# Optimization experiments

Hardware: AMD Instinct MI355X
Metric: run time of the kernel (lower is better)

## Reference

```python
import jax, jax.numpy as jnp
import numpy as np

N_NODES = 100000
N_EDGES = 3200000
B = 64            # number of graphs / RNA batch
DIM = 16          # GINE hidden dim
NFP = 33          # protein node feature dim
EMB = 128         # embedding dim
MAXLEN = 3000     # rna_global length (conv1d in_channels)
LOCLEN = 2998     # rna_local length = 3000 - log4(64) + 1
NF = 32           # n_filters
KS = 8            # conv kernel size -> 128-8+1 = 121
FC_IN = NF * 121  # 3872
BN_EPS = 1e-5


def setup_inputs() -> dict:
    key = jax.random.key(0)
    ks = jax.random.split(key, 32)
    s = 0.1
    p = {}
    # forward data args
    p['pro_x'] = jax.random.normal(ks[0], (N_NODES, NFP), jnp.float32)
    p['pro_edge_index'] = jax.random.randint(ks[1], (2, N_EDGES), 0, N_NODES, jnp.int32)
    p['pro_weight'] = jax.random.uniform(ks[2], (N_EDGES, 1), jnp.float32)
    p['pro_batch'] = jnp.sort(jax.random.randint(ks[3], (N_NODES,), 0, B, jnp.int32))
    p['rna_global'] = jax.random.randint(ks[4], (B, MAXLEN), 0, 5, jnp.int32)
    p['rna_local'] = jax.random.randint(ks[5], (B, LOCLEN), 0, 65, jnp.int32)
    # GINE layer 1 (33 -> 16)
    p['g1_w1'] = jax.random.normal(ks[6], (NFP, DIM), jnp.float32) * s
    p['g1_b1'] = jnp.zeros((DIM,), jnp.float32)
    p['g1_w2'] = jax.random.normal(ks[7], (DIM, DIM), jnp.float32) * s
    p['g1_b2'] = jnp.zeros((DIM,), jnp.float32)
    p['g1_ew'] = jax.random.normal(ks[8], (1, NFP), jnp.float32) * s  # edge Linear(1, 33)
    p['g1_eb'] = jnp.zeros((NFP,), jnp.float32)
    p['g1_eps'] = jnp.zeros((), jnp.float32)
    # GINE layers 2-5 (16 -> 16), stacked on leading axis
    p['g_w1'] = jax.random.normal(ks[9], (4, DIM, DIM), jnp.float32) * s
    p['g_b1'] = jnp.zeros((4, DIM), jnp.float32)
    p['g_w2'] = jax.random.normal(ks[10], (4, DIM, DIM), jnp.float32) * s
    p['g_b2'] = jnp.zeros((4, DIM), jnp.float32)
    p['g_ew'] = jax.random.normal(ks[11], (4, 1, DIM), jnp.float32) * s  # edge Linear(1, 16)
    p['g_eb'] = jnp.zeros((4, DIM), jnp.float32)
    p['g_eps'] = jnp.zeros((4,), jnp.float32)
    # BatchNorm1d x5
    p['bn_gamma'] = jnp.ones((5, DIM), jnp.float32)
    p['bn_beta'] = jnp.zeros((5, DIM), jnp.float32)
    # fc1_xp (16 -> 128)
    p['fc1_xp_w'] = jax.random.normal(ks[12], (DIM, EMB), jnp.float32) * s
    p['fc1_xp_b'] = jnp.zeros((EMB,), jnp.float32)
    # RNA branch
    p['emb1'] = jax.random.normal(ks[13], (5, EMB), jnp.float32)
    p['emb2'] = jax.random.normal(ks[14], (65, EMB), jnp.float32)
    p['convr1_w'] = jax.random.normal(ks[15], (NF, MAXLEN, KS), jnp.float32) * 0.01
    p['convr1_b'] = jnp.zeros((NF,), jnp.float32)
    p['convr2_w'] = jax.random.normal(ks[16], (NF, LOCLEN, KS), jnp.float32) * 0.01
    p['convr2_b'] = jnp.zeros((NF,), jnp.float32)
    p['fcxr_w'] = jax.random.normal(ks[17], (FC_IN, EMB), jnp.float32) * 0.01
    p['fcxr_b'] = jnp.zeros((EMB,), jnp.float32)
    return p


def _gine(x, src, dst, ew, w1, b1, w2, b2, ew_w, ew_b, eps):
    # GINEConv: out = MLP((1+eps)*x + sum_j relu(x_j + edge_lin(e_ij)))
    e = ew @ ew_w + ew_b                       # [E, d]
    m = jax.nn.relu(x[src] + e)                # [E, d] gather + fuse
    agg = jax.ops.segment_sum(m, dst, num_segments=N_NODES)
    h = (1.0 + eps) * x + agg
    return jax.nn.relu(h @ w1 + b1) @ w2 + b2


def _bn(x, gamma, beta):
    mu = jnp.mean(x, axis=0)
    var = jnp.var(x, axis=0)
    return (x - mu) * jax.lax.rsqrt(var + BN_EPS) * gamma + beta


def _rna_branch(tokens, emb, cw, cb, fcw, fcb):
    x = emb[tokens]                            # [B, L, 128]
    y = jax.lax.conv_general_dilated(x, cw, (1,), 'VALID',
                                     dimension_numbers=('NCH', 'OIH', 'NCH'))
    y = y + cb[None, :, None]                  # [B, 32, 121]
    return y.reshape(y.shape[0], -1) @ fcw + fcb


def reference(pro_x, pro_edge_index, pro_weight, pro_batch, rna_global, rna_local,
              g1_w1, g1_b1, g1_w2, g1_b2, g1_ew, g1_eb, g1_eps,
              g_w1, g_b1, g_w2, g_b2, g_ew, g_eb, g_eps,
              bn_gamma, bn_beta, fc1_xp_w, fc1_xp_b,
              emb1, emb2, convr1_w, convr1_b, convr2_w, convr2_b, fcxr_w, fcxr_b):
    src, dst = pro_edge_index[0], pro_edge_index[1]
    # RNA global / local branches (shared fc_xr)
    xrg = _rna_branch(rna_global, emb1, convr1_w, convr1_b, fcxr_w, fcxr_b)
    xrl = _rna_branch(rna_local, emb2, convr2_w, convr2_b, fcxr_w, fcxr_b)
    # protein GINE stack
    xp = jax.nn.relu(_gine(pro_x, src, dst, pro_weight,
                           g1_w1, g1_b1, g1_w2, g1_b2, g1_ew, g1_eb, g1_eps))
    xp = _bn(xp, bn_gamma[0], bn_beta[0])
    for i in range(4):
        xp = jax.nn.relu(_gine(xp, src, dst, pro_weight,
                               g_w1[i], g_b1[i], g_w2[i], g_b2[i],
                               g_ew[i], g_eb[i], g_eps[i]))
        xp = _bn(xp, bn_gamma[i + 1], bn_beta[i + 1])
    # global mean pool over graphs
    sums = jax.ops.segment_sum(xp, pro_batch, num_segments=B)
    cnt = jax.ops.segment_sum(jnp.ones((N_NODES, 1), xp.dtype), pro_batch, num_segments=B)
    xp = jax.nn.relu((sums / jnp.maximum(cnt, 1.0)) @ fc1_xp_w + fc1_xp_b)
    # dropout in eval mode -> identity
    xc_rna = 0.5 * (xrg + xrl)
    return (xc_rna, xp)
```

## Files before the change

kernel.cpp:

```cpp
#include <hip/hip_runtime.h>
#include <hip/hip_fp16.h>

#define N_NODES 100000
#define N_EDGES 3200000
#define BGR 64
#define DIM 16
#define NFP 33
#define ROW1 32
#define H1STR 36
#define EMB 128
#define MAXLEN 3000
#define LOCLEN 2998
#define NF 32
#define KS 8
#define OUTT 121
#define FC_IN 3872
#define BN_EPSV 1e-5f
#define POOL_CHUNK 256
#define POOL_BLKS 391
#define MLPB 391
#define AGGB1 6250
#define AGGB16 3125
#define NBIN 391
#define BCNT_BLK 512
#define P1_CHUNK 4096
#define P1_BLOCKS 782
#define MAXBIN 9088
#define NKC 32
#define KCH 121
#define WDEC (1.f / 32767.f)

__global__ void __launch_bounds__(256) k_bincnt(const int* __restrict__ dst,
                                                int* __restrict__ bh) {
    __shared__ int hist[NBIN];
    int t = threadIdx.x, bid = blockIdx.x;
    for (int b = t; b < NBIN; b += 256) hist[b] = 0;
    __syncthreads();
    int e0 = bid * (N_EDGES / BCNT_BLK);
    int e1 = e0 + (N_EDGES / BCNT_BLK);
    for (int e = e0 + t; e < e1; e += 256) atomicAdd(&hist[dst[e] >> 8], 1);
    __syncthreads();
    for (int b = t; b < NBIN; b += 256) bh[b * BCNT_BLK + bid] = hist[b];
}

__global__ void __launch_bounds__(512) k_binscan(const int* __restrict__ bh,
                                                 int* __restrict__ binoff,
                                                 int* __restrict__ bincur) {
    __shared__ int sc[512];
    int t = threadIdx.x;
    int s = 0;
    if (t < NBIN) {
        const int* row = bh + t * BCNT_BLK;
        for (int k = 0; k < BCNT_BLK; k++) s += row[k];
    }
    sc[t] = s;
    __syncthreads();
    for (int off = 1; off < 512; off <<= 1) {
        int v = (t >= off) ? sc[t - off] : 0;
        __syncthreads();
        sc[t] += v;
        __syncthreads();
    }
    int excl = sc[t] - s;
    if (t <= NBIN) binoff[t] = excl;
    if (t < NBIN) bincur[t] = excl;
}

__global__ void __launch_bounds__(256) k_part1(const int* __restrict__ src,
                                               const int* __restrict__ dst,
                                               const float* __restrict__ w,
                                               int* __restrict__ bincur,
                                               int2* __restrict__ tmp_sw) {
    __shared__ int2 srec[P1_CHUNK];
    __shared__ unsigned short sbin[P1_CHUNK];
    __shared__ unsigned short sperm[P1_CHUNK];
    __shared__ int hist[NBIN];
    __shared__ int off[NBIN];
    __shared__ int cur[NBIN];
    __shared__ int base[NBIN];
    __shared__ int sc[512];
    int t = threadIdx.x;
    int g0 = blockIdx.x * P1_CHUNK;
    int cn = N_EDGES - g0; if (cn > P1_CHUNK) cn = P1_CHUNK;
    for (int b = t; b < NBIN; b += 256) hist[b] = 0;
    __syncthreads();
    for (int j = t; j < cn; j += 256) {
        int d = dst[g0 + j];
        int b = d >> 8;
        sbin[j] = (unsigned short)b;
        srec[j] = make_int2(src[g0 + j] | ((d & 255) << 20), __float_as_int(w[g0 + j]));
        atomicAdd(&hist[b], 1);
    }
    __syncthreads();
    sc[t] = (t < NBIN) ? hist[t] : 0;
    sc[256 + t] = (256 + t < NBIN) ? hist[256 + t] : 0;
    __syncthreads();
    for (int o = 1; o <= 256; o <<= 1) {
        int v0 = (t >= o) ? sc[t - o] : 0;
        int v1 = sc[256 + t - o];
        __syncthreads();
        sc[t] += v0;
        sc[256 + t] += v1;
        __syncthreads();
    }
    for (int b = t; b < NBIN; b += 256) {
        int e = sc[b] - hist[b];
        off[b] = e;
        cur[b] = e;
        int c = hist[b];
        base[b] = c ? atomicAdd(&bincur[b], c) : 0;
    }
    __syncthreads();
    for (int j = t; j < cn; j += 256) {
        int p = atomicAdd(&cur[sbin[j]], 1);
        sperm[p] = (unsigned short)j;
    }
    __syncthreads();
    for (int p = t; p < cn; p += 256) {
        int j = sperm[p];
        int b = sbin[j];
        tmp_sw[base[b] + (p - off[b])] = srec[j];
    }
}

__global__ void __launch_bounds__(256) k_part2(const int2* __restrict__ tmp_sw,
                                               const int* __restrict__ binoff,
                                               unsigned* __restrict__ er,
                                               int* __restrict__ ptr) {
    __shared__ unsigned char sdl[MAXBIN];
    __shared__ unsigned short perm[MAXBIN];
    __shared__ int hist[256];
    __shared__ int cur[256];
    __shared__ int sc[256];
    int t = threadIdx.x, b = blockIdx.x;
    int nlo = b << 8;
    int e0 = binoff[b], e1 = binoff[b + 1];
    int cnt = e1 - e0;
    int stage = cnt < MAXBIN ? cnt : MAXBIN;
    hist[t] = 0;
    __syncthreads();
    for (int j = t; j < stage; j += 256) {
        unsigned char dl = (unsigned char)((tmp_sw[e0 + j].x >> 20) & 255);
        sdl[j] = dl;
        atomicAdd(&hist[dl], 1);
    }
    for (int j = stage + t; j < cnt; j += 256)
        atomicAdd(&hist[(tmp_sw[e0 + j].x >> 20) & 255], 1);
    __syncthreads();
    int v = hist[t];
    sc[t] = v;
    __syncthreads();
    for (int off = 1; off < 256; off <<= 1) {
        int u = (t >= off) ? sc[t - off] : 0;
        __syncthreads();
        sc[t] += u;
        __syncthreads();
    }
    int excl = sc[t] - v;
    cur[t] = excl;
    if (nlo + t < N_NODES) ptr[nlo + t] = e0 + excl;
    if (b == NBIN - 1 && t == 0) ptr[N_NODES] = N_EDGES;
    __syncthreads();
    for (int j = t; j < stage; j += 256) {
        int p = atomicAdd(&cur[sdl[j]], 1);
        perm[p] = (unsigned short)j;
    }
    __syncthreads();
    for (int j = stage + t; j < cnt; j += 256) {
        int2 sw = tmp_sw[e0 + j];
        int p = atomicAdd(&cur[(sw.x >> 20) & 255], 1);
        unsigned wq = (unsigned)(__int_as_float(sw.y) * 32767.f + 0.5f);
        er[e0 + p] = ((unsigned)sw.x & 0x1FFFFu) | (wq << 17);
    }
    for (int p = t; p < stage; p += 256) {
        int2 sw = tmp_sw[e0 + perm[p]];
        unsigned wq = (unsigned)(__int_as_float(sw.y) * 32767.f + 0.5f);
        er[e0 + p] = ((unsigned)sw.x & 0x1FFFFu) | (wq << 17);
    }
}

__global__ void k_half1(const float* __restrict__ x, __half* __restrict__ xh,
                        __half* __restrict__ xh32) {
    int i = blockIdx.x * blockDim.x + threadIdx.x;
    if (i < N_NODES * NFP) {
        int n = i / NFP, f = i - n * NFP;
        __half v = __float2half(x[i]);
        if (f < 32) xh[n * ROW1 + f] = v;
        else xh32[n] = v;
    }
}

__device__ __forceinline__ void acc8p(float a[8], uint4 r, float wv,
                                      const float* __restrict__ ewf,
                                      const float* __restrict__ ebf) {
    float2 f01 = __half22float2(*(__half2*)&r.x);
    float2 f23 = __half22float2(*(__half2*)&r.y);
    float2 f45 = __half22float2(*(__half2*)&r.z);
    float2 f67 = __half22float2(*(__half2*)&r.w);
    float x[8] = {f01.x, f01.y, f23.x, f23.y, f45.x, f45.y, f67.x, f67.y};
    #pragma unroll
    for (int j = 0; j < 8; j++)
        a[j] += fmaxf(x[j] + fmaf(wv, ewf[j], ebf[j]), 0.f);
}

__device__ __forceinline__ void acc8s(float a[8], uint4 r, float wv,
                                      const float* __restrict__ scf,
                                      const float* __restrict__ cbf,
                                      const float* __restrict__ ewf) {
    float2 f01 = __half22float2(*(__half2*)&r.x);
    float2 f23 = __half22float2(*(__half2*)&r.y);
    float2 f45 = __half22float2(*(__half2*)&r.z);
    float2 f67 = __half22float2(*(__half2*)&r.w);
    float x[8] = {f01.x, f01.y, f23.x, f23.y, f45.x, f45.y, f67.x, f67.y};
    #pragma unroll
    for (int j = 0; j < 8; j++)
        a[j] += fmaxf(fmaf(x[j], scf[j], fmaf(wv, ewf[j], cbf[j])), 0.f);
}

__global__ void __launch_bounds__(256) k_agg1(
    const __half* __restrict__ xh, const __half* __restrict__ xh32,
    const int* __restrict__ ptr, const unsigned* __restrict__ er,
    const float* __restrict__ ew, const float* __restrict__ ebv,
    const float* __restrict__ epsp, float* __restrict__ h) {
    int t = threadIdx.x;
    int wave = t >> 6, lane = t & 63;
    int nl = lane >> 4;
    int slot = (lane >> 2) & 3;
    int q = lane & 3;
    float ewf[8], ebf[8];
    #pragma unroll
    for (int j = 0; j < 8; j++) { ewf[j] = ew[q * 8 + j]; ebf[j] = ebv[q * 8 + j]; }
    float ew32 = ew[32], eb32 = ebv[32];
    float ep = 1.f + epsp[0];
    int node = blockIdx.x * 16 + wave * 4 + nl;
    int e0 = ptr[node], e1 = ptr[node + 1];
    float a[8] = {0, 0, 0, 0, 0, 0, 0, 0};
    float a32 = 0.f;
    int i = e0 + slot;
    while (i + 4 < e1) {
        unsigned ev0 = er[i];
        unsigned ev1 = er[i + 4];
        int s0 = ev0 & 0x1FFFF, s1 = ev1 & 0x1FFFF;
        float wv0 = (float)(ev0 >> 17) * WDEC;
        float wv1 = (float)(ev1 >> 17) * WDEC;
        uint4 r0 = *(const uint4*)(xh + s0 * ROW1 + q * 8);
        uint4 r1 = *(const uint4*)(xh + s1 * ROW1 + q * 8);
        acc8p(a, r0, wv0, ewf, ebf);
        acc8p(a, r1, wv1, ewf, ebf);
        if (q == 0) {
            a32 += fmaxf(__half2float(xh32[s0]) + fmaf(wv0, ew32, eb32), 0.f);
            a32 += fmaxf(__half2float(xh32[s1]) + fmaf(wv1, ew32, eb32), 0.f);
        }
        i += 8;
    }
    if (i < e1) {
        unsigned ev = er[i];
        int s = ev & 0x1FFFF;
        float wv = (float)(ev >> 17) * WDEC;
        uint4 r = *(const uint4*)(xh + s * ROW1 + q * 8);
        acc8p(a, r, wv, ewf, ebf);
        if (q == 0)
            a32 += fmaxf(__half2float(xh32[s]) + fmaf(wv, ew32, eb32), 0.f);
    }
    #pragma unroll
    for (int j = 0; j < 8; j++) {
        a[j] += __shfl_xor(a[j], 4);
        a[j] += __shfl_xor(a[j], 8);
    }
    a32 += __shfl_xor(a32, 4);
    a32 += __shfl_xor(a32, 8);
    if (slot == 0) {
        uint4 sraw = *(const uint4*)(xh + node * ROW1 + q * 8);
        float2 s01 = __half22float2(*(__half2*)&sraw.x);
        float2 s23 = __half22float2(*(__half2*)&sraw.y);
        float2 s45 = __half22float2(*(__half2*)&sraw.z);
        float2 s67 = __half22float2(*(__half2*)&sraw.w);
        float* hp = h + node * H1STR + q * 8;
        *(float4*)hp = make_float4(ep * s01.x + a[0], ep * s01.y + a[1],
                                   ep * s23.x + a[2], ep * s23.y + a[3]);
        *(float4*)(hp + 4) = make_float4(ep * s45.x + a[4], ep * s45.y + a[5],
                                         ep * s67.x + a[6], ep * s67.y + a[7]);
        if (q == 0)
            h[node * H1STR + 32] = ep * __half2float(xh32[node]) + a32;
    }
}

__global__ void __launch_bounds__(256) k_agg16(
    const __half* __restrict__ zh, const int* __restrict__ ptr,
    const unsigned* __restrict__ er,
    const float* __restrict__ ew, const float* __restrict__ ebv,
    const float* __restrict__ epsp,
    const float* __restrict__ bnstat, const float* __restrict__ gamma,
    const float* __restrict__ beta, float* __restrict__ h) {
    int t = threadIdx.x;
    int wave = t >> 6, lane = t & 63;
    int nl = lane >> 3;
    int slot = (lane >> 1) & 3;
    int hh = lane & 1;
    float ep = 1.f + epsp[0];
    const float invn = 1.f / (float)N_NODES;
    float scf[8], shf[8], cbf[8], ewf[8];
    #pragma unroll
    for (int j = 0; j < 8; j++) {
        int f = hh * 8 + j;
        float mu = bnstat[f] * invn;
        float var = bnstat[DIM + f] * invn - mu * mu;
        float sc = gamma[f] * rsqrtf(var + BN_EPSV);
        scf[j] = sc;
        shf[j] = beta[f] - mu * sc;
        cbf[j] = shf[j] + ebv[f];
        ewf[j] = ew[f];
    }
    int node = blockIdx.x * 32 + wave * 8 + nl;
    int e0 = ptr[node], e1 = ptr[node + 1];
    float a[8] = {0, 0, 0, 0, 0, 0, 0, 0};
    int i = e0 + slot;
    while (i + 4 < e1) {
        unsigned ev0 = er[i];
        unsigned ev1 = er[i + 4];
        float wv0 = (float)(ev0 >> 17) * WDEC;
        float wv1 = (float)(ev1 >> 17) * WDEC;
        uint4 r0 = *(const uint4*)(zh + (ev0 & 0x1FFFFu) * DIM + hh * 8);
        uint4 r1 = *(const uint4*)(zh + (ev1 & 0x1FFFFu) * DIM + hh * 8);
        acc8s(a, r0, wv0, scf, cbf, ewf);
        acc8s(a, r1, wv1, scf, cbf, ewf);
        i += 8;
    }
    if (i < e1) {
        unsigned ev = er[i];
        float wv = (float)(ev >> 17) * WDEC;
        uint4 r = *(const uint4*)(zh + (ev & 0x1FFFFu) * DIM + hh * 8);
        acc8s(a, r, wv, scf, cbf, ewf);
    }
    #pragma unroll
    for (int j = 0; j < 8; j++) a[j] += __shfl_xor(a[j], 2);
    #pragma unroll
    for (int j = 0; j < 8; j++) a[j] += __shfl_xor(a[j], 4);
    if (slot == 0) {
        uint4 sraw = *(const uint4*)(zh + node * DIM + hh * 8);
        float2 s01 = __half22float2(*(__half2*)&sraw.x);
        float2 s23 = __half22float2(*(__half2*)&sraw.y);
        float2 s45 = __half22float2(*(__half2*)&sraw.z);
        float2 s67 = __half22float2(*(__half2*)&sraw.w);
        float xs[8] = {s01.x, s01.y, s23.x, s23.y, s45.x, s45.y, s67.x, s67.y};
        float o8[8];
        #pragma unroll
        for (int j = 0; j < 8; j++)
            o8[j] = ep * fmaf(xs[j], scf[j], shf[j]) + a[j];
        float* hp = h + node * DIM + hh * 8;
        *(float4*)hp = make_float4(o8[0], o8[1], o8[2], o8[3]);
        *(float4*)(hp + 4) = make_float4(o8[4], o8[5], o8[6], o8[7]);
    }
}

__device__ __forceinline__ void mlp_bn_tail(float zv[16], bool active, int t,
                                            float* __restrict__ part) {
    __shared__ float red[4][32];
    float zs[16], zq[16];
    #pragma unroll
    for (int o = 0; o < 16; o++) {
        zs[o] = active ? zv[o] : 0.f;
        zq[o] = active ? zv[o] * zv[o] : 0.f;
    }
    #pragma unroll
    for (int m = 1; m <= 32; m <<= 1) {
        #pragma unroll
        for (int o = 0; o < 16; o++) {
            zs[o] += __shfl_xor(zs[o], m);
            zq[o] += __shfl_xor(zq[o], m);
        }
    }
    int wave = t >> 6, lane = t & 63;
    if (lane == 0) {
        #pragma unroll
        for (int o = 0; o < 16; o++) {
            red[wave][o] = zs[o];
            red[wave][16 + o] = zq[o];
        }
    }
    __syncthreads();
    if (t < 32)
        part[blockIdx.x * 32 + t] = red[0][t] + red[1][t] + red[2][t] + red[3][t];
}

__device__ __forceinline__ void store_zh(__half* __restrict__ zh, int n, float zv[16]) {
    __half2 p[8];
    #pragma unroll
    for (int j = 0; j < 8; j++) p[j] = __floats2half2_rn(zv[2 * j], zv[2 * j + 1]);
    *(uint4*)(zh + n * DIM) = *(uint4*)&p[0];
    *(uint4*)(zh + n * DIM + 8) = *(uint4*)&p[4];
}

__global__ void __launch_bounds__(256) k_mlp16(
    const float* __restrict__ h,
    const float* __restrict__ W1, const float* __restrict__ b1,
    const float* __restrict__ W2, const float* __restrict__ b2,
    __half* __restrict__ zh, float* __restrict__ part) {
    __shared__ float W1s[256], W2s[256], b1s[16], b2s[16];
    int t = threadIdx.x;
    W1s[t] = W1[t];
    W2s[t] = W2[t];
    if (t < 16) { b1s[t] = b1[t]; b2s[t] = b2[t]; }
    __syncthreads();
    int n = blockIdx.x * 256 + t;
    bool active = n < N_NODES;
    float zv[16];
    if (active) {
        float hv[16];
        #pragma unroll
        for (int j = 0; j < 4; j++) {
            float4 v = *(const float4*)(h + n * DIM + j * 4);
            hv[j * 4] = v.x; hv[j * 4 + 1] = v.y; hv[j * 4 + 2] = v.z; hv[j * 4 + 3] = v.w;
        }
        float tv[16];
        #pragma unroll
        for (int o = 0; o < 16; o++) {
            float s = b1s[o];
            #pragma unroll
            for (int f = 0; f < 16; f++) s += hv[f] * W1s[f * 16 + o];
            tv[o] = fmaxf(s, 0.f);
        }
        #pragma unroll
        for (int o = 0; o < 16; o++) {
            float s = b2s[o];
            #pragma unroll
            for (int f = 0; f < 16; f++) s += tv[f] * W2s[f * 16 + o];
            zv[o] = fmaxf(s, 0.f);
        }
        store_zh(zh, n, zv);
    }
    mlp_bn_tail(zv, active, t, part);
}

__global__ void __launch_bounds__(256) k_mlp1(
    const float* __restrict__ h,
    const float* __restrict__ W1, const float* __restrict__ b1,
    const float* __restrict__ W2, const float* __restrict__ b2,
    __half* __restrict__ zh, float* __restrict__ part) {
    __shared__ float W1s[NFP * 16], W2s[256], b1s[16], b2s[16];
    int t = threadIdx.x;
    for (int j = t; j < NFP * 16; j += 256) W1s[j] = W1[j];
    W2s[t] = W2[t];
    if (t < 16) { b1s[t] = b1[t]; b2s[t] = b2[t]; }
    __syncthreads();
    int n = blockIdx.x * 256 + t;
    bool active = n < N_NODES;
    float zv[16];
    if (active) {
        float hv[NFP];
        #pragma unroll
        for (int j = 0; j < 8; j++) {
            float4 v = *(const float4*)(h + n * H1STR + j * 4);
            hv[j * 4] = v.x; hv[j * 4 + 1] = v.y; hv[j * 4 + 2] = v.z; hv[j * 4 + 3] = v.w;
        }
        hv[32] = h[n * H1STR + 32];
        float tv[16];
        #pragma unroll
        for (int o = 0; o < 16; o++) {
            float s = b1s[o];
            #pragma unroll
            for (int f = 0; f < NFP; f++) s += hv[f] * W1s[f * 16 + o];
            tv[o] = fmaxf(s, 0.f);
        }
        #pragma unroll
        for (int o = 0; o < 16; o++) {
            float s = b2s[o];
            #pragma unroll
            for (int f = 0; f < 16; f++) s += tv[f] * W2s[f * 16 + o];
            zv[o] = fmaxf(s, 0.f);
        }
        store_zh(zh, n, zv);
    }
    mlp_bn_tail(zv, active, t, part);
}

__global__ void __launch_bounds__(1024) k_bnred(const float* __restrict__ part,
                                                float* __restrict__ bnstat) {
    __shared__ float red[1024];
    int t = threadIdx.x;
    int f = t & 31, g = t >> 5;
    float s = 0.f;
    for (int i = g; i < MLPB; i += 32) s += part[i * 32 + f];
    red[t] = s;
    __syncthreads();
    for (int off = 512; off >= 32; off >>= 1) {
        if (t < off) red[t] += red[t + off];
        __syncthreads();
    }
    if (t < 32) bnstat[t] = red[t];
}

__global__ void __launch_bounds__(256) k_pool(const __half* __restrict__ zh,
                                              const int* __restrict__ batch,
                                              const float* __restrict__ bnstat,
                                              const float* __restrict__ gamma,
                                              const float* __restrict__ beta,
                                              float* __restrict__ gsum,
                                              float* __restrict__ gcnt) {
    __shared__ float lsum[BGR * DIM];
    __shared__ float lcnt[BGR];
    int t = threadIdx.x;
    for (int j = t; j < BGR * DIM; j += 256) lsum[j] = 0.f;
    if (t < BGR) lcnt[t] = 0.f;
    __syncthreads();
    int f = t & 15, r = t >> 4;
    const float invn = 1.f / (float)N_NODES;
    float mu = bnstat[f] * invn;
    float var = bnstat[DIM + f] * invn - mu * mu;
    float sc = gamma[f] * rsqrtf(var + BN_EPSV);
    float sh = beta[f] - mu * sc;
    int start = blockIdx.x * POOL_CHUNK;
    float acc = 0.f, cacc = 0.f;
    int cur = -1;
    for (int i = 0; i < POOL_CHUNK / 16; i++) {
        int n = start + r + i * 16;
        if (n >= N_NODES) break;
        int b = batch[n];
        if (b != cur) {
            if (cur >= 0) {
                atomicAdd(&lsum[cur * DIM + f], acc);
                if (f == 0) atomicAdd(&lcnt[cur], cacc);
            }
            cur = b; acc = 0.f; cacc = 0.f;
        }
        acc += fmaf(__half2float(zh[n * DIM + f]), sc, sh);
        cacc += 1.f;
    }
    if (cur >= 0) {
        atomicAdd(&lsum[cur * DIM + f], acc);
        if (f == 0) atomicAdd(&lcnt[cur], cacc);
    }
    __syncthreads();
    for (int j = t; j < BGR * DIM; j += 256) {
        float v = lsum[j];
        if (v != 0.f) atomicAdd(&gsum[j], v);
    }
    if (t < BGR) {
        float v = lcnt[t];
        if (v != 0.f) atomicAdd(&gcnt[t], v);
    }
}

__global__ void k_xp(const float* __restrict__ gsum, const float* __restrict__ gcnt,
                     const float* __restrict__ w, const float* __restrict__ bias,
                     float* __restrict__ out) {
    int b = blockIdx.x;
    int e = threadIdx.x;
    float inv = 1.f / fmaxf(gcnt[b], 1.f);
    float acc = bias[e];
    #pragma unroll
    for (int f = 0; f < DIM; f++) acc += gsum[b * DIM + f] * inv * w[f * EMB + e];
    out[b * EMB + e] = fmaxf(acc, 0.f);
}

__global__ void __launch_bounds__(256) k_bucket(const int* __restrict__ tok, int L, int V,
                                                int* __restrict__ blist,
                                                int* __restrict__ bptr) {
    __shared__ int hist[65];
    __shared__ int cursor[65];
    int b = blockIdx.x, t = threadIdx.x;
    if (t < V) hist[t] = 0;
    __syncthreads();
    for (int l = t; l < L; l += 256) atomicAdd(&hist[tok[b * L + l]], 1);
    __syncthreads();
    if (t == 0) {
        int run = 0;
        for (int v = 0; v < V; v++) {
            cursor[v] = run;
            bptr[b * (V + 1) + v] = run;
            run += hist[v];
        }
        bptr[b * (V + 1) + V] = run;
    }
    __syncthreads();
    for (int l = t; l < L; l += 256) {
        int v = tok[b * L + l];
        int p = atomicAdd(&cursor[v], 1);
        blist[b * L + p] = l;
    }
}

__global__ void __launch_bounds__(256) k_wsum(const int* __restrict__ blist,
                                              const int* __restrict__ bptr,
                                              const float* __restrict__ cw,
                                              float* __restrict__ W, int L, int V) {
    int b = blockIdx.x, v = blockIdx.y;
    int t = threadIdx.x, o = t >> 3, k = t & 7;
    int s = bptr[b * (V + 1) + v], e = bptr[b * (V + 1) + v + 1];
    __shared__ int tk[256];
    const float* cwp = cw + o * (L * KS) + k;
    float acc = 0.f;
    for (int j0 = s; j0 < e; j0 += 256) {
        int lim = e - j0; if (lim > 256) lim = 256;
        __syncthreads();
        if (t < lim) tk[t] = blist[b * L + j0 + t];
        __syncthreads();
        for (int j = 0; j < lim; j++) acc += cwp[tk[j] * KS];
    }
    W[((b * NF + o) * V + v) * KS + k] = acc;
}

__global__ void k_y(const float* __restrict__ Wg, const float* __restrict__ Wl,
                    const float* __restrict__ emb1, const float* __restrict__ emb2,
                    const float* __restrict__ cb1, const float* __restrict__ cb2,
                    float* __restrict__ yg, float* __restrict__ yl) {
    int which = blockIdx.y;
    int bo = blockIdx.x;
    int b = bo >> 5, o = bo & 31;
    int t = threadIdx.x;
    const float* W = which ? Wl : Wg;
    const float* emb = which ? emb2 : emb1;
    const float* cb = which ? cb2 : cb1;
    float* y = which ? yl : yg;
    int V = which ? 65 : 5;
    __shared__ float Wsh[65 * KS];
    const float* Wrow = W + (b * NF + o) * V * KS;
    for (int j = t; j < V * KS; j += 128) Wsh[j] = Wrow[j];
    __syncthreads();
    if (t < OUTT) {
        float acc = cb[o];
        for (int v = 0; v < V; v++) {
            const float* ep = emb + v * EMB + t;
            #pragma unroll
            for (int k = 0; k < KS; k++) acc += Wsh[v * KS + k] * ep[k];
        }
        y[(b * NF + o) * OUTT + t] = acc;
    }
}

__global__ void __launch_bounds__(128) k_fcpart(const float* __restrict__ yg,
                                                const float* __restrict__ yl,
                                                const float* __restrict__ w,
                                                float* __restrict__ partial) {
    int b = blockIdx.x, which = blockIdx.y, kc = blockIdx.z;
    const float* y = which ? yl : yg;
    int e = threadIdx.x;
    __shared__ float ych[KCH];
    int j0 = kc * KCH;
    if (e < KCH) ych[e] = y[b * FC_IN + j0 + e];
    __syncthreads();
    float acc = 0.f;
    #pragma unroll 4
    for (int jj = 0; jj < KCH; jj++) acc += ych[jj] * w[(j0 + jj) * EMB + e];
    partial[((which * BGR + b) * NKC + kc) * EMB + e] = acc;
}

__global__ void k_fcred(const float* __restrict__ partial, const float* __restrict__ bias,
                        float* __restrict__ out) {
    int b = blockIdx.x;
    int e = threadIdx.x;
    const float* pg = partial + b * NKC * EMB + e;
    const float* pl = partial + (BGR + b) * NKC * EMB + e;
    float ag = bias[e], al = bias[e];
    #pragma unroll
    for (int k = 0; k < NKC; k++) { ag += pg[k * EMB]; al += pl[k * EMB]; }
    out[b * EMB + e] = 0.5f * (ag + al);
}

extern "C" void kernel_launch(void* const* d_in, const int* in_sizes, int n_in,
                              void* d_out, int out_size, void* d_ws, size_t ws_size,
                              hipStream_t stream) {
    const float* pro_x = (const float*)d_in[0];
    const int* eidx = (const int*)d_in[1];
    const int* esrc = eidx;
    const int* edst = eidx + N_EDGES;
    const float* pw = (const float*)d_in[2];
    const int* batch = (const int*)d_in[3];
    const int* rg = (const int*)d_in[4];
    const int* rl = (const int*)d_in[5];
    const float* g1_w1 = (const float*)d_in[6];
    const float* g1_b1 = (const float*)d_in[7];
    const float* g1_w2 = (const float*)d_in[8];
    const float* g1_b2 = (const float*)d_in[9];
    const float* g1_ew = (const float*)d_in[10];
    const float* g1_eb = (const float*)d_in[11];
    const float* g1_eps = (const float*)d_in[12];
    const float* g_w1 = (const float*)d_in[13];
    const float* g_b1 = (const float*)d_in[14];
    const float* g_w2 = (const float*)d_in[15];
    const float* g_b2 = (const float*)d_in[16];
    const float* g_ew = (const float*)d_in[17];
    const float* g_eb = (const float*)d_in[18];
    const float* g_eps = (const float*)d_in[19];
    const float* bn_gamma = (const float*)d_in[20];
    const float* bn_beta = (const float*)d_in[21];
    const float* fc1_xp_w = (const float*)d_in[22];
    const float* fc1_xp_b = (const float*)d_in[23];
    const float* emb1 = (const float*)d_in[24];
    const float* emb2 = (const float*)d_in[25];
    const float* convr1_w = (const float*)d_in[26];
    const float* convr1_b = (const float*)d_in[27];
    const float* convr2_w = (const float*)d_in[28];
    const float* convr2_b = (const float*)d_in[29];
    const float* fcxr_w = (const float*)d_in[30];
    const float* fcxr_b = (const float*)d_in[31];
    float* out = (float*)d_out;

    float* wsf = (float*)d_ws;
    int* ptr       = (int*)wsf;        wsf += 100128;
    int* binoff    = (int*)wsf;        wsf += 512;
    int* bincur    = (int*)wsf;        wsf += 512;
    unsigned* er   = (unsigned*)wsf;   wsf += 2 * N_EDGES;
    float* stats   = wsf;              wsf += 1280;
    float* un = wsf;
    int2* tmp_sw          = (int2*)un;
    int* bh               = (int*)(un + 7200000);
    __half* zh   = (__half*)(un + 1600000);
    __half* xh1  = (__half*)(un + 2400000);
    __half* xh32 = (__half*)(un + 4000000);
    float* bpart = un + 4100000;
    float* Wg    = un + 4300000;
    float* Wl    = un + 4382000;
    float* yg    = un + 5447000;
    float* yl    = un + 5695000;
    int* blg     = (int*)(un + 5961000);
    int* bll     = (int*)(un + 6153000);
    int* bpg     = (int*)(un + 6345000);
    int* bpl     = (int*)(un + 6346000);
    float* fcpart = un + 6360000;
    float* h      = un + 7400000;
    float* gsum   = stats;
    float* gcnt   = stats + 1024;
    float* bnstat = stats + 1088;

    hipMemsetAsync(stats, 0, 1280 * sizeof(float), stream);

    k_bincnt<<<BCNT_BLK, 256, 0, stream>>>(edst, bh);
    k_binscan<<<1, 512, 0, stream>>>(bh, binoff, bincur);
    k_part1<<<P1_BLOCKS, 256, 0, stream>>>(esrc, edst, pw, bincur, tmp_sw);
    k_part2<<<NBIN, 256, 0, stream>>>(tmp_sw, binoff, er, ptr);

    k_half1<<<(N_NODES * NFP + 255) / 256, 256, 0, stream>>>(pro_x, xh1, xh32);

    k_bucket<<<BGR, 256, 0, stream>>>(rg, MAXLEN, 5, blg, bpg);
    k_bucket<<<BGR, 256, 0, stream>>>(rl, LOCLEN, 65, bll, bpl);
    k_wsum<<<dim3(BGR, 5), 256, 0, stream>>>(blg, bpg, convr1_w, Wg, MAXLEN, 5);
    k_wsum<<<dim3(BGR, 65), 256, 0, stream>>>(bll, bpl, convr2_w, Wl, LOCLEN, 65);
    k_y<<<dim3(BGR * NF, 2), 128, 0, stream>>>(Wg, Wl, emb1, emb2, convr1_b, convr2_b, yg, yl);
    k_fcpart<<<dim3(BGR, 2, NKC), 128, 0, stream>>>(yg, yl, fcxr_w, fcpart);
    k_fcred<<<BGR, 128, 0, stream>>>(fcpart, fcxr_b, out);

    k_agg1<<<AGGB1, 256, 0, stream>>>(xh1, xh32, ptr, er, g1_ew, g1_eb, g1_eps, h);
    k_mlp1<<<MLPB, 256, 0, stream>>>(h, g1_w1, g1_b1, g1_w2, g1_b2, zh, bpart);
    k_bnred<<<1, 1024, 0, stream>>>(bpart, bnstat);
    for (int i = 0; i < 4; i++) {
        k_agg16<<<AGGB16, 256, 0, stream>>>(zh, ptr, er,
                                            g_ew + i * DIM, g_eb + i * DIM, g_eps + i,
                                            bnstat + i * 32, bn_gamma + i * DIM,
                                            bn_beta + i * DIM, h);
        k_mlp16<<<MLPB, 256, 0, stream>>>(h, g_w1 + i * DIM * DIM, g_b1 + i * DIM,
                                          g_w2 + i * DIM * DIM, g_b2 + i * DIM, zh, bpart);
        k_bnred<<<1, 1024, 0, stream>>>(bpart, bnstat + (i + 1) * 32);
    }
    k_pool<<<POOL_BLKS, 256, 0, stream>>>(zh, batch, bnstat + 4 * 32,
                                          bn_gamma + 4 * DIM, bn_beta + 4 * DIM, gsum, gcnt);
    k_xp<<<BGR, EMB, 0, stream>>>(gsum, gcnt, fc1_xp_w, fc1_xp_b, out + BGR * EMB);
}
```

Before: 645.1 us.

## Transpose conv weights for coalesced wsum, unroll edge gathers, vectorize bin scan

Adds a kernel that transposes each RNA conv weight tensor so position l holds its 256 (filter, tap) values together. k_wsum then reads one contiguous row per token, which coalesces what used to be a strided gather and removes the shared-memory staging and barriers. The GINE aggregation loops go from two to four edges in flight per lane so more gathers overlap, and the bin scan reads its rows as int4. The cost is two extra transpose launches touching about 0.77M floats each, stored in scratch space that tmp_sw uses earlier, which relies on the partition step having already finished with it.

```diff
diff --git a/kernel.cpp b/kernel.cpp
--- a/kernel.cpp
+++ b/kernel.cpp
@@ -50,8 +50,12 @@
     int t = threadIdx.x;
     int s = 0;
     if (t < NBIN) {
-        const int* row = bh + t * BCNT_BLK;
-        for (int k = 0; k < BCNT_BLK; k++) s += row[k];
+        const int4* row = (const int4*)(bh + t * BCNT_BLK);
+        #pragma unroll 4
+        for (int k = 0; k < BCNT_BLK / 4; k++) {
+            int4 v = row[k];
+            s += v.x + v.y + v.z + v.w;
+        }
     }
     sc[t] = s;
     __syncthreads();
@@ -190,6 +194,13 @@
     }
 }
 
+__global__ void __launch_bounds__(256) k_cwt(const float* __restrict__ cw,
+                                             float* __restrict__ cwT, int L) {
+    int l = blockIdx.x;
+    int ok = threadIdx.x;
+    cwT[l * 256 + ok] = cw[(ok >> 3) * (L * KS) + l * KS + (ok & 7)];
+}
+
 __device__ __forceinline__ void acc8p(float a[8], uint4 r, float wv,
                                       const float* __restrict__ ewf,
                                       const float* __restrict__ ebf) {
@@ -237,23 +248,31 @@
     float a[8] = {0, 0, 0, 0, 0, 0, 0, 0};
     float a32 = 0.f;
     int i = e0 + slot;
-    while (i + 4 < e1) {
-        unsigned ev0 = er[i];
-        unsigned ev1 = er[i + 4];
+    while (i + 12 < e1) {
+        unsigned ev0 = er[i], ev1 = er[i + 4], ev2 = er[i + 8], ev3 = er[i + 12];
         int s0 = ev0 & 0x1FFFF, s1 = ev1 & 0x1FFFF;
+        int s2 = ev2 & 0x1FFFF, s3 = ev3 & 0x1FFFF;
         float wv0 = (float)(ev0 >> 17) * WDEC;
         float wv1 = (float)(ev1 >> 17) * WDEC;
+        float wv2 = (float)(ev2 >> 17) * WDEC;
+        float wv3 = (float)(ev3 >> 17) * WDEC;
         uint4 r0 = *(const uint4*)(xh + s0 * ROW1 + q * 8);
         uint4 r1 = *(const uint4*)(xh + s1 * ROW1 + q * 8);
+        uint4 r2 = *(const uint4*)(xh + s2 * ROW1 + q * 8);
+        uint4 r3 = *(const uint4*)(xh + s3 * ROW1 + q * 8);
         acc8p(a, r0, wv0, ewf, ebf);
         acc8p(a, r1, wv1, ewf, ebf);
+        acc8p(a, r2, wv2, ewf, ebf);
+        acc8p(a, r3, wv3, ewf, ebf);
         if (q == 0) {
             a32 += fmaxf(__half2float(xh32[s0]) + fmaf(wv0, ew32, eb32), 0.f);
             a32 += fmaxf(__half2float(xh32[s1]) + fmaf(wv1, ew32, eb32), 0.f);
-        }
-        i += 8;
-    }
-    if (i < e1) {
+            a32 += fmaxf(__half2float(xh32[s2]) + fmaf(wv2, ew32, eb32), 0.f);
+            a32 += fmaxf(__half2float(xh32[s3]) + fmaf(wv3, ew32, eb32), 0.f);
+        }
+        i += 16;
+    }
+    while (i < e1) {
         unsigned ev = er[i];
         int s = ev & 0x1FFFF;
         float wv = (float)(ev >> 17) * WDEC;
@@ -261,6 +280,7 @@
         acc8p(a, r, wv, ewf, ebf);
         if (q == 0)
             a32 += fmaxf(__half2float(xh32[s]) + fmaf(wv, ew32, eb32), 0.f);
+        i += 4;
     }
     #pragma unroll
     for (int j = 0; j < 8; j++) {
@@ -315,22 +335,28 @@
     int e0 = ptr[node], e1 = ptr[node + 1];
     float a[8] = {0, 0, 0, 0, 0, 0, 0, 0};
     int i = e0 + slot;
-    while (i + 4 < e1) {
-        unsigned ev0 = er[i];
-        unsigned ev1 = er[i + 4];
+    while (i + 12 < e1) {
+        unsigned ev0 = er[i], ev1 = er[i + 4], ev2 = er[i + 8], ev3 = er[i + 12];
         float wv0 = (float)(ev0 >> 17) * WDEC;
         float wv1 = (float)(ev1 >> 17) * WDEC;
+        float wv2 = (float)(ev2 >> 17) * WDEC;
+        float wv3 = (float)(ev3 >> 17) * WDEC;
         uint4 r0 = *(const uint4*)(zh + (ev0 & 0x1FFFFu) * DIM + hh * 8);
         uint4 r1 = *(const uint4*)(zh + (ev1 & 0x1FFFFu) * DIM + hh * 8);
+        uint4 r2 = *(const uint4*)(zh + (ev2 & 0x1FFFFu) * DIM + hh * 8);
+        uint4 r3 = *(const uint4*)(zh + (ev3 & 0x1FFFFu) * DIM + hh * 8);
         acc8s(a, r0, wv0, scf, cbf, ewf);
         acc8s(a, r1, wv1, scf, cbf, ewf);
-        i += 8;
-    }
-    if (i < e1) {
+        acc8s(a, r2, wv2, scf, cbf, ewf);
+        acc8s(a, r3, wv3, scf, cbf, ewf);
+        i += 16;
+    }
+    while (i < e1) {
         unsigned ev = er[i];
         float wv = (float)(ev >> 17) * WDEC;
         uint4 r = *(const uint4*)(zh + (ev & 0x1FFFFu) * DIM + hh * 8);
         acc8s(a, r, wv, scf, cbf, ewf);
+        i += 4;
     }
     #pragma unroll
     for (int j = 0; j < 8; j++) a[j] += __shfl_xor(a[j], 2);
@@ -582,21 +608,28 @@
 
 __global__ void __launch_bounds__(256) k_wsum(const int* __restrict__ blist,
                                               const int* __restrict__ bptr,
-                                              const float* __restrict__ cw,
+                                              const float* __restrict__ cwT,
                                               float* __restrict__ W, int L, int V) {
     int b = blockIdx.x, v = blockIdx.y;
-    int t = threadIdx.x, o = t >> 3, k = t & 7;
+    int t = threadIdx.x;
     int s = bptr[b * (V + 1) + v], e = bptr[b * (V + 1) + v + 1];
-    __shared__ int tk[256];
-    const float* cwp = cw + o * (L * KS) + k;
+    const int* bl = blist + b * L;
     float acc = 0.f;
-    for (int j0 = s; j0 < e; j0 += 256) {
-        int lim = e - j0; if (lim > 256) lim = 256;
-        __syncthreads();
-        if (t < lim) tk[t] = blist[b * L + j0 + t];
-        __syncthreads();
-        for (int j = 0; j < lim; j++) acc += cwp[tk[j] * KS];
-    }
+    int j = s;
+    while (j + 3 < e) {
+        int t0 = bl[j], t1 = bl[j + 1], t2 = bl[j + 2], t3 = bl[j + 3];
+        float a0 = cwT[t0 * 256 + t];
+        float a1 = cwT[t1 * 256 + t];
+        float a2 = cwT[t2 * 256 + t];
+        float a3 = cwT[t3 * 256 + t];
+        acc += a0 + a1 + a2 + a3;
+        j += 4;
+    }
+    while (j < e) {
+        acc += cwT[bl[j] * 256 + t];
+        j++;
+    }
+    int o = t >> 3, k = t & 7;
     W[((b * NF + o) * V + v) * KS + k] = acc;
 }
 
@@ -705,6 +738,8 @@
     float* un = wsf;
     int2* tmp_sw          = (int2*)un;
     int* bh               = (int*)(un + 7200000);
+    float* cwTg  = un;
+    float* cwTl  = un + 768000;
     __half* zh   = (__half*)(un + 1600000);
     __half* xh1  = (__half*)(un + 2400000);
     __half* xh32 = (__half*)(un + 4000000);
@@ -730,12 +765,15 @@
     k_part1<<<P1_BLOCKS, 256, 0, stream>>>(esrc, edst, pw, bincur, tmp_sw);
     k_part2<<<NBIN, 256, 0, stream>>>(tmp_sw, binoff, er, ptr);
 
+    k_cwt<<<MAXLEN, 256, 0, stream>>>(convr1_w, cwTg, MAXLEN);
+    k_cwt<<<LOCLEN, 256, 0, stream>>>(convr2_w, cwTl, LOCLEN);
+
     k_half1<<<(N_NODES * NFP + 255) / 256, 256, 0, stream>>>(pro_x, xh1, xh32);
 
     k_bucket<<<BGR, 256, 0, stream>>>(rg, MAXLEN, 5, blg, bpg);
     k_bucket<<<BGR, 256, 0, stream>>>(rl, LOCLEN, 65, bll, bpl);
-    k_wsum<<<dim3(BGR, 5), 256, 0, stream>>>(blg, bpg, convr1_w, Wg, MAXLEN, 5);
-    k_wsum<<<dim3(BGR, 65), 256, 0, stream>>>(bll, bpl, convr2_w, Wl, LOCLEN, 65);
+    k_wsum<<<dim3(BGR, 5), 256, 0, stream>>>(blg, bpg, cwTg, Wg, MAXLEN, 5);
+    k_wsum<<<dim3(BGR, 65), 256, 0, stream>>>(bll, bpl, cwTl, Wl, LOCLEN, 65);
     k_y<<<dim3(BGR * NF, 2), 128, 0, stream>>>(Wg, Wl, emb1, emb2, convr1_b, convr2_b, yg, yl);
     k_fcpart<<<dim3(BGR, 2, NKC), 128, 0, stream>>>(yg, yl, fcxr_w, fcpart);
     k_fcred<<<BGR, 128, 0, stream>>>(fcpart, fcxr_b, out);
```

Measured after the change: 649.2 us. Within noise of the previous version (+0.6%).
